# Optimization experiments

Hardware: AMD Instinct MI355X
Metric: run time of the kernel (lower is better)

## Reference

```python
import jax, jax.numpy as jnp
import numpy as np

# Each of the 16 soft binary logic ops is a polynomial c0 + c1*a + c2*b + c3*a*b.
# Rows below are the [c0, c1, c2, c3] coefficients for ops 0..15 (same math as bin_op).
_OP_COEF = np.array([
    [0., 0., 0., 0.],   # 0: zeros
    [0., 0., 0., 1.],   # 1: a*b
    [0., 1., 0., -1.],  # 2: a - a*b
    [0., 1., 0., 0.],   # 3: a
    [0., 0., 1., -1.],  # 4: b - a*b
    [0., 0., 1., 0.],   # 5: b
    [0., 1., 1., -2.],  # 6: a + b - 2ab
    [0., 1., 1., -1.],  # 7: a + b - ab
    [1., -1., -1., 1.], # 8: 1 - (a + b - ab)
    [1., -1., -1., 2.], # 9: 1 - (a + b - 2ab)
    [1., 0., -1., 0.],  # 10: 1 - b
    [1., 0., -1., 1.],  # 11: 1 - b + ab
    [1., -1., 0., 0.],  # 12: 1 - a
    [1., -1., 0., 1.],  # 13: 1 - a + ab
    [1., 0., 0., -1.],  # 14: 1 - a*b
    [1., 0., 0., 0.],   # 15: ones
], dtype=np.float32)

K_CLASSES = 10
TAU = 30.0


def logic_layer(x, w, idx_a, idx_b):
    # x: [B, in_dim], w: [out_dim, 16], idx_a/idx_b: [out_dim]
    probs = jax.nn.softmax(w, axis=-1)                 # [O, 16]
    coef = probs @ jnp.asarray(_OP_COEF)               # [O, 4]
    a = x[:, idx_a]                                    # [B, O]
    b = x[:, idx_b]                                    # [B, O]
    # weighted mixture of 16 ops == polynomial in (1, a, b, a*b)
    return coef[:, 0] + coef[:, 1] * a + coef[:, 2] * b + coef[:, 3] * (a * b)


def group_sum(x, k, tau):
    B = x.shape[0]
    return x.reshape(B, k, x.shape[-1] // k).sum(-1) / tau


def setup_inputs() -> dict:
    key = jax.random.key(0)
    ks = jax.random.split(key, 10)
    B, D0, D1, D2, D3 = 4096, 1024, 8192, 8192, 10240
    return {
        "x": jax.random.uniform(ks[0], (B, D0), dtype=jnp.float32),
        "w1": jax.random.normal(ks[1], (D1, 16), dtype=jnp.float32),
        "w2": jax.random.normal(ks[2], (D2, 16), dtype=jnp.float32),
        "w3": jax.random.normal(ks[3], (D3, 16), dtype=jnp.float32),
        "idx_a1": jax.random.randint(ks[4], (D1,), 0, D0, dtype=jnp.int32),
        "idx_b1": jax.random.randint(ks[5], (D1,), 0, D0, dtype=jnp.int32),
        "idx_a2": jax.random.randint(ks[6], (D2,), 0, D1, dtype=jnp.int32),
        "idx_b2": jax.random.randint(ks[7], (D2,), 0, D1, dtype=jnp.int32),
        "idx_a3": jax.random.randint(ks[8], (D3,), 0, D2, dtype=jnp.int32),
        "idx_b3": jax.random.randint(ks[9], (D3,), 0, D2, dtype=jnp.int32),
    }


def reference(x, w1, w2, w3, idx_a1, idx_b1, idx_a2, idx_b2, idx_a3, idx_b3):
    h = logic_layer(x, w1, idx_a1, idx_b1)
    h = logic_layer(h, w2, idx_a2, idx_b2)
    h = logic_layer(h, w3, idx_a3, idx_b3)
    return group_sum(h, K_CLASSES, TAU)   # [B, 10]
```

## Files before the change

### kernel.cpp

```cpp
#include <hip/hip_runtime.h>
#include <hip/hip_fp16.h>
#include <stdint.h>

#define D0 1024
#define D1 8192
#define D2 8192
#define D3 10240
#define NGATES (D1 + D2 + D3)
#define B_ROWS 4096

#define SMEM_H1    0
#define SMEM_H2    65536
#define SMEM_XB    131072
#define SMEM_CSUM  139264
#define SMEM_BYTES (139264 + 160)

__global__ __launch_bounds__(64) void prep_kernel(
    const float* __restrict__ w1, const float* __restrict__ w2,
    const float* __restrict__ w3,
    const int* __restrict__ ia1, const int* __restrict__ ib1,
    const int* __restrict__ ia2, const int* __restrict__ ib2,
    const int* __restrict__ ia3, const int* __restrict__ ib3,
    uint4* __restrict__ coefb, uint32_t* __restrict__ idxp) {
    int G = blockIdx.x * 64 + threadIdx.x;
    const float* w;
    int ia, ib;
    if (G < D1) {
        w = w1 + (size_t)G * 16; ia = ia1[G]; ib = ib1[G];
    } else if (G < D1 + D2) {
        int g = G - D1;
        w = w2 + (size_t)g * 16; ia = ia2[g]; ib = ib2[g];
    } else {
        int g = G - D1 - D2;
        w = w3 + (size_t)g * 16; ia = ia3[g]; ib = ib3[g];
    }
    const float4* wv = (const float4*)w;
    float4 q0 = wv[0], q1 = wv[1], q2 = wv[2], q3 = wv[3];
    float wa[16] = {q0.x, q0.y, q0.z, q0.w, q1.x, q1.y, q1.z, q1.w,
                    q2.x, q2.y, q2.z, q2.w, q3.x, q3.y, q3.z, q3.w};
    float m = wa[0];
#pragma unroll
    for (int i = 1; i < 16; ++i) m = fmaxf(m, wa[i]);
    float e[16], s = 0.f;
#pragma unroll
    for (int i = 0; i < 16; ++i) { e[i] = __expf(wa[i] - m); s += e[i]; }
    float inv = 1.f / s;
    static constexpr float OPC[16][4] = {
        {0.f, 0.f, 0.f, 0.f}, {0.f, 0.f, 0.f, 1.f}, {0.f, 1.f, 0.f, -1.f}, {0.f, 1.f, 0.f, 0.f},
        {0.f, 0.f, 1.f, -1.f}, {0.f, 0.f, 1.f, 0.f}, {0.f, 1.f, 1.f, -2.f}, {0.f, 1.f, 1.f, -1.f},
        {1.f, -1.f, -1.f, 1.f}, {1.f, -1.f, -1.f, 2.f}, {1.f, 0.f, -1.f, 0.f}, {1.f, 0.f, -1.f, 1.f},
        {1.f, -1.f, 0.f, 0.f}, {1.f, -1.f, 0.f, 1.f}, {1.f, 0.f, 0.f, -1.f}, {1.f, 0.f, 0.f, 0.f}};
    float c0 = 0.f, c1 = 0.f, c2 = 0.f, c3 = 0.f;
#pragma unroll
    for (int i = 0; i < 16; ++i) {
        float p = e[i] * inv;
        c0 += p * OPC[i][0];
        c1 += p * OPC[i][1];
        c2 += p * OPC[i][2];
        c3 += p * OPC[i][3];
    }
    uint4 cv;
    cv.x = __builtin_bit_cast(uint32_t, __floats2half2_rn(c0, c0));
    cv.y = __builtin_bit_cast(uint32_t, __floats2half2_rn(c1, c1));
    cv.z = __builtin_bit_cast(uint32_t, __floats2half2_rn(c2, c2));
    cv.w = __builtin_bit_cast(uint32_t, __floats2half2_rn(c3, c3));
    coefb[G] = cv;
    idxp[G] = (uint32_t)(ia << 3) | ((uint32_t)(ib << 3) << 16);
}

__device__ __forceinline__ uint2 gate4(uint2 av, uint2 bv, uint4 cf) {
    __half2 a01 = __builtin_bit_cast(__half2, av.x);
    __half2 a23 = __builtin_bit_cast(__half2, av.y);
    __half2 b01 = __builtin_bit_cast(__half2, bv.x);
    __half2 b23 = __builtin_bit_cast(__half2, bv.y);
    __half2 c0 = __builtin_bit_cast(__half2, cf.x);
    __half2 c1 = __builtin_bit_cast(__half2, cf.y);
    __half2 c2 = __builtin_bit_cast(__half2, cf.z);
    __half2 c3 = __builtin_bit_cast(__half2, cf.w);
    __half2 h01 = __hfma2(a01, __hfma2(b01, c3, c1), __hfma2(b01, c2, c0));
    __half2 h23 = __hfma2(a23, __hfma2(b23, c3, c1), __hfma2(b23, c2, c0));
    uint2 r;
    r.x = __builtin_bit_cast(uint32_t, h01);
    r.y = __builtin_bit_cast(uint32_t, h23);
    return r;
}

__global__ __launch_bounds__(1024) void fused_kernel(
    const float* __restrict__ x, const uint4* __restrict__ coefb,
    const uint32_t* __restrict__ idxp, float* __restrict__ out) {
    extern __shared__ char smem[];
    char* sm = smem;
    uint2* h1 = (uint2*)(sm + SMEM_H1);
    uint2* h2 = (uint2*)(sm + SMEM_H2);
    uint2* xb = (uint2*)(sm + SMEM_XB);
    float* csum = (float*)(sm + SMEM_CSUM);

    const int t = threadIdx.x;
    const int rowbase = blockIdx.x << 2;

    uint32_t pI[8];
    uint4 pC[8];
#pragma unroll
    for (int k = 0; k < 8; ++k) {
        int g = t + (k << 10);
        pI[k] = idxp[g];
        pC[k] = coefb[g];
    }

    {
        const float* xp = x + (size_t)rowbase * D0 + t;
        float v0 = xp[0];
        float v1 = xp[D0];
        float v2 = xp[2 * D0];
        float v3 = xp[3 * D0];
        uint2 v;
        v.x = __builtin_bit_cast(uint32_t, __floats2half2_rn(v0, v1));
        v.y = __builtin_bit_cast(uint32_t, __floats2half2_rn(v2, v3));
        xb[t] = v;
    }
    if (t < 40) csum[t] = 0.f;
    __syncthreads();

#pragma unroll
    for (int k = 0; k < 8; ++k) {
        int g = t + (k << 10);
        uint32_t ip = pI[k];
        uint2 av = *(const uint2*)(sm + SMEM_XB + (ip & 0xffffu));
        uint2 bv = *(const uint2*)(sm + SMEM_XB + (ip >> 16));
        h1[g] = gate4(av, bv, pC[k]);
    }
#pragma unroll
    for (int k = 0; k < 8; ++k) {
        int g = D1 + t + (k << 10);
        pI[k] = idxp[g];
        pC[k] = coefb[g];
    }
    __syncthreads();

#pragma unroll
    for (int k = 0; k < 8; ++k) {
        int g = t + (k << 10);
        uint32_t ip = pI[k];
        uint2 av = *(const uint2*)(sm + (ip & 0xffffu));
        uint2 bv = *(const uint2*)(sm + (ip >> 16));
        h2[g] = gate4(av, bv, pC[k]);
    }
    __syncthreads();

    {
        const int wv = t >> 6, lane = t & 63;
        const int gbase = wv * 640;
        const int cA = gbase >> 10;
        const int bnd = (cA + 1) << 10;
        float s0[4] = {0.f, 0.f, 0.f, 0.f};
        float s1[4] = {0.f, 0.f, 0.f, 0.f};
#pragma unroll
        for (int j = 0; j < 10; ++j) {
            int gc = gbase + (j << 6);
            int g = D1 + D2 + gc + lane;
            uint32_t ip = idxp[g];
            uint4 cf = coefb[g];
            uint2 av = *(const uint2*)(sm + SMEM_H2 + (ip & 0xffffu));
            uint2 bv = *(const uint2*)(sm + SMEM_H2 + (ip >> 16));
            uint2 hv = gate4(av, bv, cf);
            __half2 h01 = __builtin_bit_cast(__half2, hv.x);
            __half2 h23 = __builtin_bit_cast(__half2, hv.y);
            float f0 = __low2float(h01), f1 = __high2float(h01);
            float f2 = __low2float(h23), f3 = __high2float(h23);
            if (gc < bnd) {
                s0[0] += f0; s0[1] += f1; s0[2] += f2; s0[3] += f3;
            } else {
                s1[0] += f0; s1[1] += f1; s1[2] += f2; s1[3] += f3;
            }
        }
#pragma unroll
        for (int m = 1; m < 64; m <<= 1) {
#pragma unroll
            for (int r = 0; r < 4; ++r) {
                s0[r] += __shfl_xor(s0[r], m, 64);
                s1[r] += __shfl_xor(s1[r], m, 64);
            }
        }
        if (lane == 0) {
#pragma unroll
            for (int r = 0; r < 4; ++r) atomicAdd(&csum[cA * 4 + r], s0[r]);
            if (gbase + 640 > bnd) {
#pragma unroll
                for (int r = 0; r < 4; ++r) atomicAdd(&csum[(cA + 1) * 4 + r], s1[r]);
            }
        }
    }
    __syncthreads();

    if (t < 40) {
        int c = t >> 2, r = t & 3;
        out[(size_t)(rowbase + r) * 10 + c] = csum[t] * (1.0f / 30.0f);
    }
}

extern "C" void kernel_launch(void* const* d_in, const int* in_sizes, int n_in,
                              void* d_out, int out_size, void* d_ws, size_t ws_size,
                              hipStream_t stream) {
    const float* x = (const float*)d_in[0];
    const float* w1 = (const float*)d_in[1];
    const float* w2 = (const float*)d_in[2];
    const float* w3 = (const float*)d_in[3];
    const int* ia1 = (const int*)d_in[4];
    const int* ib1 = (const int*)d_in[5];
    const int* ia2 = (const int*)d_in[6];
    const int* ib2 = (const int*)d_in[7];
    const int* ia3 = (const int*)d_in[8];
    const int* ib3 = (const int*)d_in[9];
    float* out = (float*)d_out;

    uint4* coefb = (uint4*)d_ws;
    uint32_t* idxp = (uint32_t*)((char*)d_ws + (size_t)NGATES * 16);

    hipFuncSetAttribute(reinterpret_cast<const void*>(fused_kernel),
                        hipFuncAttributeMaxDynamicSharedMemorySize, SMEM_BYTES);

    prep_kernel<<<NGATES / 64, 64, 0, stream>>>(
        w1, w2, w3, ia1, ib1, ia2, ib2, ia3, ib3, coefb, idxp);
    fused_kernel<<<B_ROWS / 4, 1024, SMEM_BYTES, stream>>>(x, coefb, idxp, out);
}
```

Baseline: 114.1 us.

## Split fused kernel into two kernels to cut LDS per block

Splits the single fused kernel into one kernel for layers 1-2 and one for layer 3 plus the group sum. The layer-2 output now goes through a global workspace buffer instead of shared memory. Each kernel needs much less LDS, so more blocks can be resident per CU to hide gather latency. In exchange it adds a global write and read of the intermediate activations and one extra kernel launch.

```diff
diff --git a/kernel.cpp b/kernel.cpp
--- a/kernel.cpp
+++ b/kernel.cpp
@@ -9,11 +9,11 @@
 #define NGATES (D1 + D2 + D3)
 #define B_ROWS 4096
 
-#define SMEM_H1    0
-#define SMEM_H2    65536
-#define SMEM_XB    131072
-#define SMEM_CSUM  139264
-#define SMEM_BYTES (139264 + 160)
+#define SM1_H1    0
+#define SM1_XB    65536
+#define SM1_BYTES 73728
+#define SM2_CSUM  65536
+#define SM2_BYTES (65536 + 160)
 
 __global__ __launch_bounds__(64) void prep_kernel(
     const float* __restrict__ w1, const float* __restrict__ w2,
@@ -85,15 +85,12 @@
     return r;
 }
 
-__global__ __launch_bounds__(1024) void fused_kernel(
+__global__ __launch_bounds__(1024, 8) void k1_layers12(
     const float* __restrict__ x, const uint4* __restrict__ coefb,
-    const uint32_t* __restrict__ idxp, float* __restrict__ out) {
-    extern __shared__ char smem[];
-    char* sm = smem;
-    uint2* h1 = (uint2*)(sm + SMEM_H1);
-    uint2* h2 = (uint2*)(sm + SMEM_H2);
-    uint2* xb = (uint2*)(sm + SMEM_XB);
-    float* csum = (float*)(sm + SMEM_CSUM);
+    const uint32_t* __restrict__ idxp, uint2* __restrict__ h2g) {
+    extern __shared__ char sm[];
+    uint2* h1 = (uint2*)(sm + SM1_H1);
+    uint2* xb = (uint2*)(sm + SM1_XB);
 
     const int t = threadIdx.x;
     const int rowbase = blockIdx.x << 2;
@@ -118,15 +115,14 @@
         v.y = __builtin_bit_cast(uint32_t, __floats2half2_rn(v2, v3));
         xb[t] = v;
     }
-    if (t < 40) csum[t] = 0.f;
     __syncthreads();
 
 #pragma unroll
     for (int k = 0; k < 8; ++k) {
         int g = t + (k << 10);
         uint32_t ip = pI[k];
-        uint2 av = *(const uint2*)(sm + SMEM_XB + (ip & 0xffffu));
-        uint2 bv = *(const uint2*)(sm + SMEM_XB + (ip >> 16));
+        uint2 av = *(const uint2*)(sm + SM1_XB + (ip & 0xffffu));
+        uint2 bv = *(const uint2*)(sm + SM1_XB + (ip >> 16));
         h1[g] = gate4(av, bv, pC[k]);
     }
 #pragma unroll
@@ -137,14 +133,33 @@
     }
     __syncthreads();
 
+    uint2* h2out = h2g + ((size_t)blockIdx.x << 13);
 #pragma unroll
     for (int k = 0; k < 8; ++k) {
         int g = t + (k << 10);
         uint32_t ip = pI[k];
         uint2 av = *(const uint2*)(sm + (ip & 0xffffu));
         uint2 bv = *(const uint2*)(sm + (ip >> 16));
-        h2[g] = gate4(av, bv, pC[k]);
-    }
+        h2out[g] = gate4(av, bv, pC[k]);
+    }
+}
+
+__global__ __launch_bounds__(1024, 8) void k2_layer3(
+    const uint2* __restrict__ h2g, const uint4* __restrict__ coefb,
+    const uint32_t* __restrict__ idxp, float* __restrict__ out) {
+    extern __shared__ char sm[];
+    float* csum = (float*)(sm + SM2_CSUM);
+
+    const int t = threadIdx.x;
+    const int rowbase = blockIdx.x << 2;
+
+    {
+        uint4* dst = (uint4*)sm;
+        const uint4* src = (const uint4*)(h2g + ((size_t)blockIdx.x << 13));
+#pragma unroll
+        for (int j = 0; j < 4; ++j) dst[t + (j << 10)] = src[t + (j << 10)];
+    }
+    if (t < 40) csum[t] = 0.f;
     __syncthreads();
 
     {
@@ -160,8 +175,8 @@
             int g = D1 + D2 + gc + lane;
             uint32_t ip = idxp[g];
             uint4 cf = coefb[g];
-            uint2 av = *(const uint2*)(sm + SMEM_H2 + (ip & 0xffffu));
-            uint2 bv = *(const uint2*)(sm + SMEM_H2 + (ip >> 16));
+            uint2 av = *(const uint2*)(sm + (ip & 0xffffu));
+            uint2 bv = *(const uint2*)(sm + (ip >> 16));
             uint2 hv = gate4(av, bv, cf);
             __half2 h01 = __builtin_bit_cast(__half2, hv.x);
             __half2 h23 = __builtin_bit_cast(__half2, hv.y);
@@ -215,11 +230,15 @@
 
     uint4* coefb = (uint4*)d_ws;
     uint32_t* idxp = (uint32_t*)((char*)d_ws + (size_t)NGATES * 16);
-
-    hipFuncSetAttribute(reinterpret_cast<const void*>(fused_kernel),
-                        hipFuncAttributeMaxDynamicSharedMemorySize, SMEM_BYTES);
+    uint2* h2g = (uint2*)((char*)d_ws + (size_t)NGATES * 20 + 4096);
+
+    hipFuncSetAttribute(reinterpret_cast<const void*>(k1_layers12),
+                        hipFuncAttributeMaxDynamicSharedMemorySize, SM1_BYTES);
+    hipFuncSetAttribute(reinterpret_cast<const void*>(k2_layer3),
+                        hipFuncAttributeMaxDynamicSharedMemorySize, SM2_BYTES);
 
     prep_kernel<<<NGATES / 64, 64, 0, stream>>>(
         w1, w2, w3, ia1, ib1, ia2, ib2, ia3, ib3, coefb, idxp);
-    fused_kernel<<<B_ROWS / 4, 1024, SMEM_BYTES, stream>>>(x, coefb, idxp, out);
-}
+    k1_layers12<<<B_ROWS / 4, 1024, SM1_BYTES, stream>>>(x, coefb, idxp, h2g);
+    k2_layer3<<<B_ROWS / 4, 1024, SM2_BYTES, stream>>>(h2g, coefb, idxp, out);
+}
```

New measurement: 120.6 us. +5.7%, slower.

## Recompute layer-1 gates inline within layer 2 to drop h1 from shared memory

Applied to the files above, without the earlier changes.

The prep kernel now emits, for each layer-2 gate, the x indices and coefficients of its two layer-1 parents. The fused kernel can then compute layer-1 outputs on the fly from x and skip the h1 buffer in shared memory. This cuts LDS from about 139KB to about 74KB, so two 1024-thread blocks can share a CU, and it removes one barrier. Coefficients are also packed as fp16 pairs (8 bytes instead of 16). In exchange layer-1 gates are recomputed (two per layer-2 gate instead of one shared result), with four random LDS reads per gate.

```diff
diff --git a/kernel.cpp b/kernel.cpp
--- a/kernel.cpp
+++ b/kernel.cpp
@@ -6,34 +6,14 @@
 #define D1 8192
 #define D2 8192
 #define D3 10240
-#define NGATES (D1 + D2 + D3)
 #define B_ROWS 4096
 
-#define SMEM_H1    0
-#define SMEM_H2    65536
-#define SMEM_XB    131072
-#define SMEM_CSUM  139264
-#define SMEM_BYTES (139264 + 160)
-
-__global__ __launch_bounds__(64) void prep_kernel(
-    const float* __restrict__ w1, const float* __restrict__ w2,
-    const float* __restrict__ w3,
-    const int* __restrict__ ia1, const int* __restrict__ ib1,
-    const int* __restrict__ ia2, const int* __restrict__ ib2,
-    const int* __restrict__ ia3, const int* __restrict__ ib3,
-    uint4* __restrict__ coefb, uint32_t* __restrict__ idxp) {
-    int G = blockIdx.x * 64 + threadIdx.x;
-    const float* w;
-    int ia, ib;
-    if (G < D1) {
-        w = w1 + (size_t)G * 16; ia = ia1[G]; ib = ib1[G];
-    } else if (G < D1 + D2) {
-        int g = G - D1;
-        w = w2 + (size_t)g * 16; ia = ia2[g]; ib = ib2[g];
-    } else {
-        int g = G - D1 - D2;
-        w = w3 + (size_t)g * 16; ia = ia3[g]; ib = ib3[g];
-    }
+#define SM_XB     0
+#define SM_H2     8192
+#define SM_CSUM   (8192 + 65536)
+#define SM_BYTES  (8192 + 65536 + 160)
+
+__device__ __forceinline__ float4 softmax_coef(const float* __restrict__ w) {
     const float4* wv = (const float4*)w;
     float4 q0 = wv[0], q1 = wv[1], q2 = wv[2], q3 = wv[3];
     float wa[16] = {q0.x, q0.y, q0.z, q0.w, q1.x, q1.y, q1.z, q1.w,
@@ -59,24 +39,56 @@
         c2 += p * OPC[i][2];
         c3 += p * OPC[i][3];
     }
-    uint4 cv;
-    cv.x = __builtin_bit_cast(uint32_t, __floats2half2_rn(c0, c0));
-    cv.y = __builtin_bit_cast(uint32_t, __floats2half2_rn(c1, c1));
-    cv.z = __builtin_bit_cast(uint32_t, __floats2half2_rn(c2, c2));
-    cv.w = __builtin_bit_cast(uint32_t, __floats2half2_rn(c3, c3));
-    coefb[G] = cv;
-    idxp[G] = (uint32_t)(ia << 3) | ((uint32_t)(ib << 3) << 16);
-}
-
-__device__ __forceinline__ uint2 gate4(uint2 av, uint2 bv, uint4 cf) {
+    return make_float4(c0, c1, c2, c3);
+}
+
+__device__ __forceinline__ uint2 pack_coef(float4 c) {
+    uint2 r;
+    r.x = __builtin_bit_cast(uint32_t, __floats2half2_rn(c.x, c.y));
+    r.y = __builtin_bit_cast(uint32_t, __floats2half2_rn(c.z, c.w));
+    return r;
+}
+
+__global__ __launch_bounds__(64) void prep_kernel(
+    const float* __restrict__ w1, const float* __restrict__ w2,
+    const float* __restrict__ w3,
+    const int* __restrict__ ia1, const int* __restrict__ ib1,
+    const int* __restrict__ ia2, const int* __restrict__ ib2,
+    const int* __restrict__ ia3, const int* __restrict__ ib3,
+    uint2* __restrict__ bcIdx, uint4* __restrict__ bcCoefAB,
+    uint2* __restrict__ bcCoefO, uint32_t* __restrict__ d3Idx,
+    uint2* __restrict__ d3Coef) {
+    int G = blockIdx.x * 64 + threadIdx.x;
+    if (G < D2) {
+        int g = G;
+        int pa = ia2[g], pb = ib2[g];
+        float4 cO = softmax_coef(w2 + (size_t)g * 16);
+        float4 cA = softmax_coef(w1 + (size_t)pa * 16);
+        float4 cB = softmax_coef(w1 + (size_t)pb * 16);
+        uint2 xi;
+        xi.x = (uint32_t)(ia1[pa] << 3) | ((uint32_t)(ib1[pa] << 3) << 16);
+        xi.y = (uint32_t)(ia1[pb] << 3) | ((uint32_t)(ib1[pb] << 3) << 16);
+        bcIdx[g] = xi;
+        uint2 a = pack_coef(cA), b = pack_coef(cB);
+        bcCoefAB[g] = make_uint4(a.x, a.y, b.x, b.y);
+        bcCoefO[g] = pack_coef(cO);
+    } else {
+        int g = G - D2;
+        float4 cO = softmax_coef(w3 + (size_t)g * 16);
+        d3Idx[g] = (uint32_t)(ia3[g] << 3) | ((uint32_t)(ib3[g] << 3) << 16);
+        d3Coef[g] = pack_coef(cO);
+    }
+}
+
+__device__ __forceinline__ uint2 gate4(uint2 av, uint2 bv, uint2 cf) {
+    __half2 p = __builtin_bit_cast(__half2, cf.x);
+    __half2 q = __builtin_bit_cast(__half2, cf.y);
+    __half2 c0 = __low2half2(p), c1 = __high2half2(p);
+    __half2 c2 = __low2half2(q), c3 = __high2half2(q);
     __half2 a01 = __builtin_bit_cast(__half2, av.x);
     __half2 a23 = __builtin_bit_cast(__half2, av.y);
     __half2 b01 = __builtin_bit_cast(__half2, bv.x);
     __half2 b23 = __builtin_bit_cast(__half2, bv.y);
-    __half2 c0 = __builtin_bit_cast(__half2, cf.x);
-    __half2 c1 = __builtin_bit_cast(__half2, cf.y);
-    __half2 c2 = __builtin_bit_cast(__half2, cf.z);
-    __half2 c3 = __builtin_bit_cast(__half2, cf.w);
     __half2 h01 = __hfma2(a01, __hfma2(b01, c3, c1), __hfma2(b01, c2, c0));
     __half2 h23 = __hfma2(a23, __hfma2(b23, c3, c1), __hfma2(b23, c2, c0));
     uint2 r;
@@ -85,27 +97,18 @@
     return r;
 }
 
-__global__ __launch_bounds__(1024) void fused_kernel(
-    const float* __restrict__ x, const uint4* __restrict__ coefb,
-    const uint32_t* __restrict__ idxp, float* __restrict__ out) {
-    extern __shared__ char smem[];
-    char* sm = smem;
-    uint2* h1 = (uint2*)(sm + SMEM_H1);
-    uint2* h2 = (uint2*)(sm + SMEM_H2);
-    uint2* xb = (uint2*)(sm + SMEM_XB);
-    float* csum = (float*)(sm + SMEM_CSUM);
+__global__ __launch_bounds__(1024, 8) void fused_kernel(
+    const float* __restrict__ x, const uint2* __restrict__ bcIdx,
+    const uint4* __restrict__ bcCoefAB, const uint2* __restrict__ bcCoefO,
+    const uint32_t* __restrict__ d3Idx, const uint2* __restrict__ d3Coef,
+    float* __restrict__ out) {
+    extern __shared__ char sm[];
+    uint2* xb = (uint2*)(sm + SM_XB);
+    uint2* h2 = (uint2*)(sm + SM_H2);
+    float* csum = (float*)(sm + SM_CSUM);
 
     const int t = threadIdx.x;
     const int rowbase = blockIdx.x << 2;
-
-    uint32_t pI[8];
-    uint4 pC[8];
-#pragma unroll
-    for (int k = 0; k < 8; ++k) {
-        int g = t + (k << 10);
-        pI[k] = idxp[g];
-        pC[k] = coefb[g];
-    }
 
     {
         const float* xp = x + (size_t)rowbase * D0 + t;
@@ -121,29 +124,18 @@
     if (t < 40) csum[t] = 0.f;
     __syncthreads();
 
-#pragma unroll
     for (int k = 0; k < 8; ++k) {
         int g = t + (k << 10);
-        uint32_t ip = pI[k];
-        uint2 av = *(const uint2*)(sm + SMEM_XB + (ip & 0xffffu));
-        uint2 bv = *(const uint2*)(sm + SMEM_XB + (ip >> 16));
-        h1[g] = gate4(av, bv, pC[k]);
-    }
-#pragma unroll
-    for (int k = 0; k < 8; ++k) {
-        int g = D1 + t + (k << 10);
-        pI[k] = idxp[g];
-        pC[k] = coefb[g];
-    }
-    __syncthreads();
-
-#pragma unroll
-    for (int k = 0; k < 8; ++k) {
-        int g = t + (k << 10);
-        uint32_t ip = pI[k];
-        uint2 av = *(const uint2*)(sm + (ip & 0xffffu));
-        uint2 bv = *(const uint2*)(sm + (ip >> 16));
-        h2[g] = gate4(av, bv, pC[k]);
+        uint2 xi = bcIdx[g];
+        uint4 cab = bcCoefAB[g];
+        uint2 co = bcCoefO[g];
+        uint2 aa = *(const uint2*)(sm + (xi.x & 0xffffu));
+        uint2 ab = *(const uint2*)(sm + (xi.x >> 16));
+        uint2 ba = *(const uint2*)(sm + (xi.y & 0xffffu));
+        uint2 bb = *(const uint2*)(sm + (xi.y >> 16));
+        uint2 ha = gate4(aa, ab, make_uint2(cab.x, cab.y));
+        uint2 hb = gate4(ba, bb, make_uint2(cab.z, cab.w));
+        h2[g] = gate4(ha, hb, co);
     }
     __syncthreads();
 
@@ -157,11 +149,11 @@
 #pragma unroll
         for (int j = 0; j < 10; ++j) {
             int gc = gbase + (j << 6);
-            int g = D1 + D2 + gc + lane;
-            uint32_t ip = idxp[g];
-            uint4 cf = coefb[g];
-            uint2 av = *(const uint2*)(sm + SMEM_H2 + (ip & 0xffffu));
-            uint2 bv = *(const uint2*)(sm + SMEM_H2 + (ip >> 16));
+            int g = gc + lane;
+            uint32_t ip = d3Idx[g];
+            uint2 cf = d3Coef[g];
+            uint2 av = *(const uint2*)(sm + SM_H2 + (ip & 0xffffu));
+            uint2 bv = *(const uint2*)(sm + SM_H2 + (ip >> 16));
             uint2 hv = gate4(av, bv, cf);
             __half2 h01 = __builtin_bit_cast(__half2, hv.x);
             __half2 h23 = __builtin_bit_cast(__half2, hv.y);
@@ -213,13 +205,19 @@
     const int* ib3 = (const int*)d_in[9];
     float* out = (float*)d_out;
 
-    uint4* coefb = (uint4*)d_ws;
-    uint32_t* idxp = (uint32_t*)((char*)d_ws + (size_t)NGATES * 16);
+    char* p = (char*)d_ws;
+    uint2* bcIdx = (uint2*)p;                 p += (size_t)D2 * 8;
+    uint4* bcCoefAB = (uint4*)p;              p += (size_t)D2 * 16;
+    uint2* bcCoefO = (uint2*)p;               p += (size_t)D2 * 8;
+    uint32_t* d3Idx = (uint32_t*)p;           p += (size_t)D3 * 4;
+    uint2* d3Coef = (uint2*)p;
 
     hipFuncSetAttribute(reinterpret_cast<const void*>(fused_kernel),
-                        hipFuncAttributeMaxDynamicSharedMemorySize, SMEM_BYTES);
-
-    prep_kernel<<<NGATES / 64, 64, 0, stream>>>(
-        w1, w2, w3, ia1, ib1, ia2, ib2, ia3, ib3, coefb, idxp);
-    fused_kernel<<<B_ROWS / 4, 1024, SMEM_BYTES, stream>>>(x, coefb, idxp, out);
-}
+                        hipFuncAttributeMaxDynamicSharedMemorySize, SM_BYTES);
+
+    prep_kernel<<<(D2 + D3) / 64, 64, 0, stream>>>(
+        w1, w2, w3, ia1, ib1, ia2, ib2, ia3, ib3,
+        bcIdx, bcCoefAB, bcCoefO, d3Idx, d3Coef);
+    fused_kernel<<<B_ROWS / 4, 1024, SM_BYTES, stream>>>(
+        x, bcIdx, bcCoefAB, bcCoefO, d3Idx, d3Coef, out);
+}
```

After: 107.1 us. -6.1%, faster.
